# Optimization experiments

Measured on AMD Instinct MI355X. Metric: run time of the kernel, lower is better.

## Reference

```python
import jax, jax.numpy as jnp
import numpy as np

IN_DIM = 512
HID = 1024
E = 16
TOPK = 2


def setup_inputs() -> dict:
    key = jax.random.key(0)
    ks = jax.random.split(key, 8)
    s = 0.02
    x = jax.random.normal(ks[0], (4, 2048, IN_DIM), dtype=jnp.float32)
    Wr = jax.random.normal(ks[1], (IN_DIM, E), dtype=jnp.float32) * s
    br = jnp.zeros((E,), dtype=jnp.float32)
    W1 = jax.random.normal(ks[2], (E, IN_DIM, HID), dtype=jnp.float32) * s
    b1 = jnp.zeros((E, HID), dtype=jnp.float32)
    W2 = jax.random.normal(ks[3], (E, HID, IN_DIM), dtype=jnp.float32) * s
    b2 = jnp.zeros((E, IN_DIM), dtype=jnp.float32)
    return {"x": x, "Wr": Wr, "br": br, "W1": W1, "b1": b1, "W2": W2, "b2": b2}


def reference(x, Wr, br, W1, b1, W2, b2):
    token_shape = x.shape[:-1]
    xf = x.reshape(-1, x.shape[-1])            # [T, D]
    T = xf.shape[0]

    # router (temperature = 1.0)
    logits = xf @ Wr + br                       # [T, E]
    probs = jax.nn.softmax(logits, axis=-1)
    topk_w, topk_idx = jax.lax.top_k(probs, TOPK)           # [T, K]
    topk_w = topk_w / jnp.maximum(topk_w.sum(-1, keepdims=True), 1e-9)

    # combine weights: [T, E], zero where not routed
    combine = jnp.zeros((T, E), dtype=xf.dtype).at[
        jnp.arange(T)[:, None], topk_idx].add(topk_w)

    # per-expert MLP (exact GELU, as torch nn.GELU default), weighted combine
    y = jnp.zeros_like(xf)
    for e in range(E):
        h = jax.nn.gelu(xf @ W1[e] + b1[e], approximate=False)  # [T, H]
        o = h @ W2[e] + b2[e]                                   # [T, D]
        y = y + combine[:, e:e + 1] * o

    # residual (in_dim == out_dim)
    y = xf + y
    return y.reshape(*token_shape, IN_DIM)
```

## Files before the change

### kernel.cpp

```cpp
#include <hip/hip_runtime.h>
#include <hip/hip_bf16.h>
#include <math.h>

#define IN_DIM 512
#define HID    1024
#define NE     16
#define T_TOK  8192
#define NPAIR  (T_TOK*2)

typedef __attribute__((ext_vector_type(8))) short bf16x8;
typedef __attribute__((ext_vector_type(4))) float f32x4;

__device__ __forceinline__ unsigned short f2b(float f){
  unsigned u = __float_as_uint(f);
  u += 0x7FFF + ((u >> 16) & 1);
  return (unsigned short)(u >> 16);
}
__device__ __forceinline__ float b2f(unsigned short u){
  return __uint_as_float(((unsigned)u) << 16);
}

__device__ __forceinline__ void barrier_lds_only(){
  asm volatile("s_waitcnt lgkmcnt(0)" ::: "memory");
  __builtin_amdgcn_s_barrier();
}

typedef const __attribute__((address_space(1))) unsigned int* gas1_t;
typedef __attribute__((address_space(3))) unsigned int* las3_t;
__device__ __forceinline__ void gl16(const unsigned short* g, unsigned short* l){
  __builtin_amdgcn_global_load_lds((gas1_t)(const void*)g, (las3_t)(void*)l, 16, 0, 0);
}

__global__ __launch_bounds__(256) void tconv2_kernel(const float* __restrict__ A1,
                                                     unsigned short* __restrict__ O1,
                                                     const float* __restrict__ A2,
                                                     unsigned short* __restrict__ O2){
  __shared__ float tile[32][33];
  int b = blockIdx.x;
  const float* src; unsigned short* dst; int M, N, m0, n0;
  if (b < 8192){
    M = IN_DIM; N = HID;
    int e = b >> 9, r = b & 511;
    n0 = (r & 31)*32; m0 = (r >> 5)*32;
    src = A1 + (size_t)e*M*N; dst = O1 + (size_t)e*M*N;
  } else {
    int b2 = b - 8192;
    M = HID; N = IN_DIM;
    int e = b2 >> 9, r = b2 & 511;
    n0 = (r & 15)*32; m0 = (r >> 4)*32;
    src = A2 + (size_t)e*M*N; dst = O2 + (size_t)e*M*N;
  }
  int c = threadIdx.x & 31, r = threadIdx.x >> 5;
  #pragma unroll
  for (int i=0;i<4;i++)
    tile[r + i*8][c] = src[(size_t)(m0 + r + i*8)*N + n0 + c];
  __syncthreads();
  int tr  = threadIdx.x >> 3;
  int tc4 = (threadIdx.x & 7) * 4;
  ushort4 o;
  o.x = f2b(tile[tc4+0][tr]); o.y = f2b(tile[tc4+1][tr]);
  o.z = f2b(tile[tc4+2][tr]); o.w = f2b(tile[tc4+3][tr]);
  *(ushort4*)(&dst[(size_t)(n0 + tr)*M + m0 + tc4]) = o;
}

__global__ __launch_bounds__(256) void router_kernel(
    const float* __restrict__ x, const float* __restrict__ Wr, const float* __restrict__ br,
    unsigned short* __restrict__ xb, int* __restrict__ eid, float* __restrict__ pw)
{
  int wid = threadIdx.x >> 6, lane = threadIdx.x & 63;
  int t = blockIdx.x*4 + wid;
  const float4* xr4 = (const float4*)(x + (size_t)t*IN_DIM);
  ushort4*      xb4 = (ushort4*)(xb + (size_t)t*IN_DIM);

  float acc[NE];
  #pragma unroll
  for (int i=0;i<NE;i++) acc[i]=0.f;

  #pragma unroll
  for (int j=0;j<2;j++){
    int f = j*64 + lane;
    float4 v = xr4[f];
    ushort4 o; o.x=f2b(v.x); o.y=f2b(v.y); o.z=f2b(v.z); o.w=f2b(v.w);
    xb4[f] = o;
    const float4* wr4 = (const float4*)(Wr + (size_t)(f*4)*NE);
    const float* vv = (const float*)&v;
    #pragma unroll
    for (int rr=0; rr<4; rr++){
      float xv = vv[rr];
      #pragma unroll
      for (int q=0;q<4;q++){
        float4 w = wr4[rr*4+q];
        acc[q*4+0] += xv*w.x; acc[q*4+1] += xv*w.y;
        acc[q*4+2] += xv*w.z; acc[q*4+3] += xv*w.w;
      }
    }
  }
  #pragma unroll
  for (int off=32; off>=1; off>>=1){
    #pragma unroll
    for (int i=0;i<NE;i++) acc[i] += __shfl_xor(acc[i], off, 64);
  }
  if (lane==0){
    #pragma unroll
    for (int i=0;i<NE;i++) acc[i] += br[i];
    int e0=0; float l0=acc[0];
    #pragma unroll
    for (int i=1;i<NE;i++) if (acc[i] > l0){ l0=acc[i]; e0=i; }
    int e1=-1; float l1=-3.0e38f;
    #pragma unroll
    for (int i=0;i<NE;i++) if (i!=e0 && acc[i] > l1){ l1=acc[i]; e1=i; }
    float w0 = 1.f/(1.f + __expf(l1 - l0));
    float w1 = 1.f - w0;
    pw[t*2+0] = w0; pw[t*2+1] = w1;
    eid[t*2+0] = e0; eid[t*2+1] = e1;
  }
}

__global__ __launch_bounds__(1024) void bucket_kernel(const int* __restrict__ eid,
                                                      int* __restrict__ cnt,
                                                      int* __restrict__ bucket){
  int e = blockIdx.x;
  __shared__ int lbase;
  if (threadIdx.x == 0) lbase = 0;
  __syncthreads();
  int lane = threadIdx.x & 63, wid = threadIdx.x >> 6;
  int* be = bucket + e*T_TOK;
  for (int c = wid*64; c < NPAIR; c += 1024){
    int p = c + lane;
    bool ok = (eid[p] == e);
    unsigned long long m = __ballot(ok);
    int rank = __popcll(m & ((1ull << lane) - 1ull));
    int count = __popcll(m);
    int base = 0;
    if (lane == 0) base = atomicAdd(&lbase, count);
    base = __shfl(base, 0, 64);
    if (ok) be[base + rank] = p;
  }
  __syncthreads();
  if (threadIdx.x == 0) cnt[e] = lbase;
}


#define STAGE(buf, kt) do{ \
      gl16(Ag0 + (kt)*32, ldsA + (buf)*4096); \
      gl16(Ag1 + (kt)*32, ldsA + (buf)*4096 + 2048); \
      gl16(Bg0 + (kt)*32, ldsB + (buf)*4096); \
      gl16(Bg1 + (kt)*32, ldsB + (buf)*4096 + 2048); \
    }while(0)

#define COMPUTE(buf) do{ \
      const unsigned short* Ac = lds + (buf)*4096; \
      const unsigned short* Bc = lds + 8192 + (buf)*4096; \
      bf16x8 af[4], bfr[4]; \
      _Pragma("unroll") \
      for (int s=0;s<4;s++) af[s]  = *(const bf16x8*)(Ac + (wm + s*16 + fr)*32 + pf8); \
      _Pragma("unroll") \
      for (int u=0;u<4;u++) bfr[u] = *(const bf16x8*)(Bc + (wn + u*16 + fr)*32 + pf8); \
      _Pragma("unroll") \
      for (int s=0;s<4;s++) \
        _Pragma("unroll") \
        for (int u=0;u<4;u++) \
          acc[s][u] = __builtin_amdgcn_mfma_f32_16x16x32_bf16(af[s], bfr[u], acc[s][u], 0,0,0); \
    }while(0)

#define KBODY(k, P) do{ \
      STAGE((P)^1, (k)+1); \
      asm volatile("s_waitcnt vmcnt(4)" ::: "memory"); \
      barrier_lds_only(); \
      COMPUTE(P); \
      barrier_lds_only(); \
    }while(0)

template<int KDIM, int NDIM, bool FIRST>
__global__ __launch_bounds__(256) void moe_gemm(
    const unsigned short* __restrict__ A,
    const unsigned short* __restrict__ Bm,
    const float* __restrict__ bias,
    const int* __restrict__ cnt,
    const int* __restrict__ bucket,
    const float* __restrict__ pw,
    unsigned short* __restrict__ hb,
    unsigned short* __restrict__ opb)
{
  constexpr int NS  = KDIM / 32;
  constexpr int NBT = NDIM / 128;

  int ntiles = 0;
  #pragma unroll
  for (int j=0;j<NE;j++) ntiles += ((cnt[j]+127)>>7)*NBT;

  __shared__ unsigned short lds[16384];

  const int tid  = threadIdx.x;
  const int lane = tid & 63, wid = tid >> 6;
  const int lr = tid >> 2;
  const int c  = tid & 3;
  const int cs = (c ^ ((lr >> 1) & 3)) * 8;
  unsigned short* ldsA = lds + wid*512;
  unsigned short* ldsB = lds + 8192 + wid*512;

  const int wm = (wid>>1)*64, wn = (wid&1)*64;
  const int fr = lane & 15, fb = lane >> 4;
  const int pf8 = (fb ^ ((fr >> 1) & 3)) * 8;
  const int fq = fb*4;

  for (int t = blockIdx.x; t < ntiles; t += gridDim.x){
    int e=0, tloc=0, ebase=0, ce=0, itl=1;
    {
      int cum=0, crow=0;
      #pragma unroll
      for (int j=0;j<NE;j++){
        int cj = cnt[j];
        int it = (cj+127)>>7;
        int tj = it * NBT;
        bool in = (t >= cum) & (t < cum+tj);
        if (in){ e=j; tloc=t-cum; ebase=crow; ce=cj; itl=it; }
        cum += tj; crow += cj;
      }
    }
    const int i0 = (tloc % itl) * 128;
    const int n0 = (tloc / itl) * 128;

    const int* buck = bucket + e*T_TOK;
    int arow0, arow1;
    if (FIRST){
      int p0 = i0 + lr, p1 = i0 + 64 + lr;
      arow0 = buck[(p0 < ce) ? p0 : i0] >> 1;
      arow1 = buck[(p1 < ce) ? p1 : i0] >> 1;
    } else {
      arow0 = ebase + i0 + lr;      if (arow0 > NPAIR-1) arow0 = NPAIR-1;
      arow1 = ebase + i0 + 64 + lr; if (arow1 > NPAIR-1) arow1 = NPAIR-1;
    }
    const unsigned short* Ag0 = A + (size_t)arow0*KDIM + cs;
    const unsigned short* Ag1 = A + (size_t)arow1*KDIM + cs;
    const unsigned short* Bg0 = Bm + (size_t)e*NDIM*KDIM + (size_t)(n0 + lr)*KDIM + cs;
    const unsigned short* Bg1 = Bg0 + (size_t)64*KDIM;

    f32x4 acc[4][4];
    #pragma unroll
    for (int s=0;s<4;s++)
      #pragma unroll
      for (int u=0;u<4;u++)
        #pragma unroll
        for (int j=0;j<4;j++) acc[s][u][j] = 0.f;

    STAGE(0, 0);
    for (int k=0; k+1 < NS-1; k+=2){ KBODY(k, 0); KBODY(k+1, 1); }
    KBODY(NS-2, 0);
    asm volatile("s_waitcnt vmcnt(0)" ::: "memory");
    barrier_lds_only();
    COMPUTE(1);
    barrier_lds_only();

    #pragma unroll
    for (int s=0;s<4;s++){
      #pragma unroll
      for (int i=0;i<4;i++){
        int row = wm + s*16 + fq + i;
        int pos = i0 + row;
        if (pos >= ce) continue;
        #pragma unroll
        for (int u=0;u<4;u++){
          int n = n0 + wn + u*16 + fr;
          float v = acc[s][u][i] + bias[e*NDIM + n];
          if (FIRST){
            float g = 0.5f*v*(1.f + erff(v*0.70710678118654752f));
            hb[(size_t)(ebase + pos)*NDIM + n] = f2b(g);
          } else {
            int pair = buck[pos];
            opb[(size_t)pair*NDIM + n] = f2b(pw[pair]*v);
          }
        }
      }
    }
  }
}

#undef KBODY
#undef COMPUTE
#undef STAGE

__global__ __launch_bounds__(256) void combine_kernel(const float* __restrict__ x,
                                                      const unsigned short* __restrict__ opb,
                                                      float* __restrict__ out){
  int i = blockIdx.x*256 + threadIdx.x;
  int t  = i >> 7;
  int c4 = i & 127;
  float4 v = ((const float4*)x)[i];
  ushort4 a = ((const ushort4*)opb)[(size_t)(2*t)*128 + c4];
  ushort4 b = ((const ushort4*)opb)[(size_t)(2*t+1)*128 + c4];
  v.x += b2f(a.x) + b2f(b.x);
  v.y += b2f(a.y) + b2f(b.y);
  v.z += b2f(a.z) + b2f(b.z);
  v.w += b2f(a.w) + b2f(b.w);
  ((float4*)out)[i] = v;
}

extern "C" void kernel_launch(void* const* d_in, const int* in_sizes, int n_in,
                              void* d_out, int out_size, void* d_ws, size_t ws_size,
                              hipStream_t stream)
{
  const float* x  = (const float*)d_in[0];
  const float* Wr = (const float*)d_in[1];
  const float* br = (const float*)d_in[2];
  const float* W1 = (const float*)d_in[3];
  const float* b1 = (const float*)d_in[4];
  const float* W2 = (const float*)d_in[5];
  const float* b2 = (const float*)d_in[6];
  float* out = (float*)d_out;
  char* ws = (char*)d_ws;

  int*            cnt    = (int*)(ws + 0);
  int*            bucket = (int*)(ws + 1024);
  float*          pw     = (float*)(ws + 525312);
  unsigned short* xb     = (unsigned short*)(ws + 590848);
  unsigned short* w1t    = (unsigned short*)(ws + 8979456);
  unsigned short* w2t    = (unsigned short*)(ws + 25756672);
  unsigned short* hb     = (unsigned short*)(ws + 42533888);
  int*            eid    = (int*)(ws + 42533888);
  unsigned short* opb    = w1t;

  router_kernel<<<T_TOK/4, 256, 0, stream>>>(x, Wr, br, xb, eid, pw);
  bucket_kernel<<<NE, 1024, 0, stream>>>(eid, cnt, bucket);
  tconv2_kernel<<<16384, 256, 0, stream>>>(W1, w1t, W2, w2t);
  moe_gemm<IN_DIM, HID, true ><<<1024, 256, 0, stream>>>(
      xb, w1t, b1, cnt, bucket, pw, hb, opb);
  moe_gemm<HID, IN_DIM, false><<<1024, 256, 0, stream>>>(
      hb, w2t, b2, cnt, bucket, pw, hb, opb);
  combine_kernel<<<(T_TOK*IN_DIM/4)/256, 256, 0, stream>>>(x, opb, out);
}
```

Measured before the change: 286.7 us.

## Enlarge MoE GEMM tiles to 256-row blocks with BK=64 and 512-thread workgroups

Reworks the grouped expert GEMM to use 256-row M tiles, BK=64 K steps, templated N tile and wave grid (256x256 for the first GEMM, 256x128 for the second), and 512-thread blocks with an XOR-swizzled LDS layout. The K loop becomes a single-barrier double-buffered loop with s_setprio around the MFMA section. The tile index is remapped across blocks, and the per-row pair and weight loads are hoisted out of the epilogue. Larger tiles are meant to raise arithmetic intensity and cut LDS and global traffic per FLOP. In exchange there is more padding waste for partially filled expert tiles, higher register and LDS pressure, and fewer tiles to spread across CUs.

```diff
diff --git a/kernel.cpp b/kernel.cpp
--- a/kernel.cpp
+++ b/kernel.cpp
@@ -141,38 +141,36 @@
 }
 
 
-#define STAGE(buf, kt) do{ \
-      gl16(Ag0 + (kt)*32, ldsA + (buf)*4096); \
-      gl16(Ag1 + (kt)*32, ldsA + (buf)*4096 + 2048); \
-      gl16(Bg0 + (kt)*32, ldsB + (buf)*4096); \
-      gl16(Bg1 + (kt)*32, ldsB + (buf)*4096 + 2048); \
+#define STAGE(BUF, KT) do{ \
+      _Pragma("unroll") \
+      for (int j=0;j<4;j++) \
+        gl16(Ag[j] + (KT)*BK, lds + (BUF)*ASZ + wid*2048 + j*512); \
+      _Pragma("unroll") \
+      for (int j=0;j<NBJ_B;j++) \
+        gl16(Bg[j] + (KT)*BK, lds + 2*ASZ + (BUF)*BSZ + wid*(NBJ_B*512) + j*512); \
     }while(0)
 
-#define COMPUTE(buf) do{ \
-      const unsigned short* Ac = lds + (buf)*4096; \
-      const unsigned short* Bc = lds + 8192 + (buf)*4096; \
-      bf16x8 af[4], bfr[4]; \
+#define COMPUTE(BUF) do{ \
+      const unsigned short* lcA = lds + (BUF)*ASZ; \
+      const unsigned short* lcB = lds + 2*ASZ + (BUF)*BSZ; \
       _Pragma("unroll") \
-      for (int s=0;s<4;s++) af[s]  = *(const bf16x8*)(Ac + (wm + s*16 + fr)*32 + pf8); \
-      _Pragma("unroll") \
-      for (int u=0;u<4;u++) bfr[u] = *(const bf16x8*)(Bc + (wn + u*16 + fr)*32 + pf8); \
-      _Pragma("unroll") \
-      for (int s=0;s<4;s++) \
+      for (int kk=0; kk<2; kk++){ \
+        const int ch = ((kk*4 + fb) ^ (fr & 7)) * 8; \
+        bf16x8 af[SA], bfr[SU]; \
         _Pragma("unroll") \
-        for (int u=0;u<4;u++) \
-          acc[s][u] = __builtin_amdgcn_mfma_f32_16x16x32_bf16(af[s], bfr[u], acc[s][u], 0,0,0); \
+        for (int s=0;s<SA;s++) af[s]  = *(const bf16x8*)(lcA + (wm + s*16 + fr)*BK + ch); \
+        _Pragma("unroll") \
+        for (int u=0;u<SU;u++) bfr[u] = *(const bf16x8*)(lcB + (wn + u*16 + fr)*BK + ch); \
+        _Pragma("unroll") \
+        for (int s=0;s<SA;s++) \
+          _Pragma("unroll") \
+          for (int u=0;u<SU;u++) \
+            acc[s][u] = __builtin_amdgcn_mfma_f32_16x16x32_bf16(af[s], bfr[u], acc[s][u], 0,0,0); \
+      } \
     }while(0)
 
-#define KBODY(k, P) do{ \
-      STAGE((P)^1, (k)+1); \
-      asm volatile("s_waitcnt vmcnt(4)" ::: "memory"); \
-      barrier_lds_only(); \
-      COMPUTE(P); \
-      barrier_lds_only(); \
-    }while(0)
-
-template<int KDIM, int NDIM, bool FIRST>
-__global__ __launch_bounds__(256) void moe_gemm(
+template<int KDIM, int NDIM, int BN, int WGN, bool FIRST>
+__global__ __launch_bounds__(512, 2) void moe_gemm(
     const unsigned short* __restrict__ A,
     const unsigned short* __restrict__ Bm,
     const float* __restrict__ bias,
@@ -182,93 +180,111 @@
     unsigned short* __restrict__ hb,
     unsigned short* __restrict__ opb)
 {
-  constexpr int NS  = KDIM / 32;
-  constexpr int NBT = NDIM / 128;
+  constexpr int BK  = 64;
+  constexpr int NS  = KDIM / BK;
+  constexpr int NBT = NDIM / BN;
+  constexpr int WGM = 8 / WGN;
+  constexpr int SA  = (256/WGM)/16;
+  constexpr int SU  = (BN/WGN)/16;
+  constexpr int ASZ = 256*BK;
+  constexpr int BSZ = BN*BK;
+  constexpr int NBJ_B = BN/64;
 
   int ntiles = 0;
   #pragma unroll
-  for (int j=0;j<NE;j++) ntiles += ((cnt[j]+127)>>7)*NBT;
-
-  __shared__ unsigned short lds[16384];
+  for (int j=0;j<NE;j++) ntiles += ((cnt[j]+255)>>8)*NBT;
+
+  __shared__ unsigned short lds[2*ASZ + 2*BSZ];
 
   const int tid  = threadIdx.x;
   const int lane = tid & 63, wid = tid >> 6;
-  const int lr = tid >> 2;
-  const int c  = tid & 3;
-  const int cs = (c ^ ((lr >> 1) & 3)) * 8;
-  unsigned short* ldsA = lds + wid*512;
-  unsigned short* ldsB = lds + 8192 + wid*512;
-
-  const int wm = (wid>>1)*64, wn = (wid&1)*64;
-  const int fr = lane & 15, fb = lane >> 4;
-  const int pf8 = (fb ^ ((fr >> 1) & 3)) * 8;
-  const int fq = fb*4;
-
-  for (int t = blockIdx.x; t < ntiles; t += gridDim.x){
+  const int rsub = lane >> 3;
+  const int cs   = ((lane & 7) ^ rsub) * 8;
+  const int fr = lane & 15, fb = lane >> 4, fq = fb*4;
+  const int wm = (wid / WGN) * (256/WGM);
+  const int wn = (wid % WGN) * (BN/WGN);
+
+  for (int t = (blockIdx.x & 7)*64 + (blockIdx.x >> 3); t < ntiles; t += gridDim.x){
     int e=0, tloc=0, ebase=0, ce=0, itl=1;
     {
       int cum=0, crow=0;
       #pragma unroll
       for (int j=0;j<NE;j++){
         int cj = cnt[j];
-        int it = (cj+127)>>7;
+        int it = (cj+255)>>8;
         int tj = it * NBT;
         bool in = (t >= cum) & (t < cum+tj);
         if (in){ e=j; tloc=t-cum; ebase=crow; ce=cj; itl=it; }
         cum += tj; crow += cj;
       }
     }
-    const int i0 = (tloc % itl) * 128;
-    const int n0 = (tloc / itl) * 128;
+    const int i0 = (tloc % itl) * 256;
+    const int n0 = (tloc / itl) * BN;
 
     const int* buck = bucket + e*T_TOK;
-    int arow0, arow1;
-    if (FIRST){
-      int p0 = i0 + lr, p1 = i0 + 64 + lr;
-      arow0 = buck[(p0 < ce) ? p0 : i0] >> 1;
-      arow1 = buck[(p1 < ce) ? p1 : i0] >> 1;
-    } else {
-      arow0 = ebase + i0 + lr;      if (arow0 > NPAIR-1) arow0 = NPAIR-1;
-      arow1 = ebase + i0 + 64 + lr; if (arow1 > NPAIR-1) arow1 = NPAIR-1;
-    }
-    const unsigned short* Ag0 = A + (size_t)arow0*KDIM + cs;
-    const unsigned short* Ag1 = A + (size_t)arow1*KDIM + cs;
-    const unsigned short* Bg0 = Bm + (size_t)e*NDIM*KDIM + (size_t)(n0 + lr)*KDIM + cs;
-    const unsigned short* Bg1 = Bg0 + (size_t)64*KDIM;
-
-    f32x4 acc[4][4];
-    #pragma unroll
-    for (int s=0;s<4;s++)
+    const unsigned short* Ag[4];
+    #pragma unroll
+    for (int j=0;j<4;j++){
+      int p = i0 + wid*32 + j*8 + rsub;
+      int arow;
+      if (FIRST){
+        arow = buck[(p < ce) ? p : i0] >> 1;
+      } else {
+        arow = ebase + p; if (arow > NPAIR-1) arow = NPAIR-1;
+      }
+      Ag[j] = A + (size_t)arow*KDIM + cs;
+    }
+    const unsigned short* Bg[NBJ_B];
+    #pragma unroll
+    for (int j=0;j<NBJ_B;j++)
+      Bg[j] = Bm + (size_t)e*NDIM*KDIM + (size_t)(n0 + wid*(NBJ_B*8) + j*8 + rsub)*KDIM + cs;
+
+    f32x4 acc[SA][SU];
+    #pragma unroll
+    for (int s=0;s<SA;s++)
       #pragma unroll
-      for (int u=0;u<4;u++)
+      for (int u=0;u<SU;u++)
         #pragma unroll
         for (int j=0;j<4;j++) acc[s][u][j] = 0.f;
 
     STAGE(0, 0);
-    for (int k=0; k+1 < NS-1; k+=2){ KBODY(k, 0); KBODY(k+1, 1); }
-    KBODY(NS-2, 0);
     asm volatile("s_waitcnt vmcnt(0)" ::: "memory");
     barrier_lds_only();
-    COMPUTE(1);
+    int cur = 0;
+    #pragma unroll 1
+    for (int kt=0; kt<NS-1; ++kt){
+      STAGE(cur^1, kt+1);
+      __builtin_amdgcn_s_setprio(1);
+      COMPUTE(cur);
+      __builtin_amdgcn_s_setprio(0);
+      asm volatile("s_waitcnt vmcnt(0)" ::: "memory");
+      barrier_lds_only();
+      cur ^= 1;
+    }
+    __builtin_amdgcn_s_setprio(1);
+    COMPUTE(cur);
+    __builtin_amdgcn_s_setprio(0);
     barrier_lds_only();
 
-    #pragma unroll
-    for (int s=0;s<4;s++){
+    const float* be = bias + e*NDIM;
+    #pragma unroll
+    for (int s=0;s<SA;s++){
       #pragma unroll
       for (int i=0;i<4;i++){
         int row = wm + s*16 + fq + i;
         int pos = i0 + row;
         if (pos >= ce) continue;
+        int pair = 0; float pwv = 0.f;
+        if (!FIRST){ pair = buck[pos]; pwv = pw[pair]; }
         #pragma unroll
-        for (int u=0;u<4;u++){
+        for (int u=0;u<SU;u++){
           int n = n0 + wn + u*16 + fr;
-          float v = acc[s][u][i] + bias[e*NDIM + n];
+          float v = acc[s][u][i] + be[n];
           if (FIRST){
             float g = 0.5f*v*(1.f + erff(v*0.70710678118654752f));
             hb[(size_t)(ebase + pos)*NDIM + n] = f2b(g);
           } else {
-            int pair = buck[pos];
-            opb[(size_t)pair*NDIM + n] = f2b(pw[pair]*v);
+            opb[(size_t)pair*NDIM + n] = f2b(pwv*v);
           }
         }
       }
@@ -276,7 +292,6 @@
   }
 }
 
-#undef KBODY
 #undef COMPUTE
 #undef STAGE
 
@@ -323,9 +338,9 @@
   router_kernel<<<T_TOK/4, 256, 0, stream>>>(x, Wr, br, xb, eid, pw);
   bucket_kernel<<<NE, 1024, 0, stream>>>(eid, cnt, bucket);
   tconv2_kernel<<<16384, 256, 0, stream>>>(W1, w1t, W2, w2t);
-  moe_gemm<IN_DIM, HID, true ><<<1024, 256, 0, stream>>>(
+  moe_gemm<IN_DIM, HID, 256, 4, true ><<<512, 512, 0, stream>>>(
       xb, w1t, b1, cnt, bucket, pw, hb, opb);
-  moe_gemm<HID, IN_DIM, false><<<1024, 256, 0, stream>>>(
+  moe_gemm<HID, IN_DIM, 128, 2, false><<<512, 512, 0, stream>>>(
       hb, w2t, b2, cnt, bucket, pw, hb, opb);
   combine_kernel<<<(T_TOK*IN_DIM/4)/256, 256, 0, stream>>>(x, opb, out);
 }
```

After: 294.6 us. 2.8% more time.
